# Kernel optimization log

Hardware: AMD Instinct MI355X
Metric: run time of the kernel (lower is better)

Reference implementation:

```python
import jax, jax.numpy as jnp
import numpy as np

N_NODES = 100000
N_EDGES = 1600000
D_IN = 128
HID = 128
E_CH = 16


def setup_inputs() -> dict:
    key = jax.random.key(0)
    ks = jax.random.split(key, 16)

    def glorot(k, shape):
        fan_in, fan_out = shape[0], shape[1]
        lim = jnp.sqrt(6.0 / (fan_in + fan_out))
        return jax.random.uniform(k, shape, jnp.float32, -lim, lim)

    inp = {
        "x": jax.random.normal(ks[0], (N_NODES, D_IN), jnp.float32),
        "edge_index": jax.random.randint(ks[1], (2, N_EDGES), 0, N_NODES, jnp.int32),
        "edge_attr": jax.random.normal(ks[2], (N_EDGES, E_CH), jnp.float32),
        # SAGEConv layer 0: lin_l (neighbor agg, with bias), lin_r (root, no bias)
        "Wl0": glorot(ks[3], (D_IN, HID)),
        "Wr0": glorot(ks[4], (D_IN, HID)),
        "b0": jnp.zeros((HID,), jnp.float32),
        # SAGEConv layer 1
        "Wl1": glorot(ks[5], (HID, HID)),
        "Wr1": glorot(ks[6], (HID, HID)),
        "b1": jnp.zeros((HID,), jnp.float32),
        # classifier MLP: (2*HID + E_CH) -> 128 -> 64 -> 1
        "Wc1": glorot(ks[7], (2 * HID + E_CH, 128)),
        "bc1": jnp.zeros((128,), jnp.float32),
        "Wc2": glorot(ks[8], (128, 64)),
        "bc2": jnp.zeros((64,), jnp.float32),
        "Wc3": glorot(ks[9], (64, 1)),
        "bc3": jnp.zeros((1,), jnp.float32),
    }
    return inp


def _sage_conv(x, src, dst, Wl, Wr, b):
    # PyG SAGEConv (aggr='mean'): out = lin_l(mean_j x_j) + lin_r(x_i)
    # messages flow src -> dst
    msg_sum = jax.ops.segment_sum(x[src], dst, num_segments=N_NODES)  # [N, D]
    deg = jax.ops.segment_sum(jnp.ones((src.shape[0],), x.dtype), dst,
                              num_segments=N_NODES)                   # [N]
    agg = msg_sum / jnp.maximum(deg, 1.0)[:, None]  # mean; isolated nodes -> 0
    return agg @ Wl + b + x @ Wr


def reference(x, edge_index, edge_attr,
              Wl0, Wr0, b0, Wl1, Wr1, b1,
              Wc1, bc1, Wc2, bc2, Wc3, bc3):
    src, dst = edge_index[0], edge_index[1]
    # encode: two SAGEConv layers, each followed by ReLU (dropout is identity at eval)
    h = jax.nn.relu(_sage_conv(x, src, dst, Wl0, Wr0, b0))
    h = jax.nn.relu(_sage_conv(h, src, dst, Wl1, Wr1, b1))
    # edge classifier: gather endpoint embeddings, concat edge features
    feat = jnp.concatenate([h[src], h[dst], edge_attr], axis=-1)  # [E, 2H+EC]
    z = jax.nn.relu(feat @ Wc1 + bc1)
    z = jax.nn.relu(z @ Wc2 + bc2)
    logits = (z @ Wc3 + bc3).reshape(-1)  # [E]
    return jax.nn.sigmoid(logits)
```

## Files before the change

### kernel.cpp

```cpp
#include <hip/hip_runtime.h>
#include <hip/hip_bf16.h>
#include <math.h>

#define NN 100000
#define NE 1600000
#define NBLK 391
#define ZSTRIDE 296

typedef __bf16 bf16x8 __attribute__((ext_vector_type(8)));
typedef float f32x4 __attribute__((ext_vector_type(4)));

union BF8 { bf16x8 v; unsigned short u[8]; };

static __device__ __forceinline__ unsigned short f2bf(float f) {
  unsigned int u = __float_as_uint(f);
  unsigned int r = u + 0x7fffu + ((u >> 16) & 1u);
  return (unsigned short)(r >> 16);
}
static __device__ __forceinline__ f32x4 zero4() {
  f32x4 z = {0.f, 0.f, 0.f, 0.f}; return z;
}
static __device__ __forceinline__ bf16x8 zerobf8() {
  BF8 t;
  #pragma unroll
  for (int j = 0; j < 8; ++j) t.u[j] = 0;
  return t.v;
}
static __device__ __forceinline__ bf16x8 cvt8(float4 v0, float4 v1, float s) {
  BF8 t;
  t.u[0]=f2bf(v0.x*s); t.u[1]=f2bf(v0.y*s); t.u[2]=f2bf(v0.z*s); t.u[3]=f2bf(v0.w*s);
  t.u[4]=f2bf(v1.x*s); t.u[5]=f2bf(v1.y*s); t.u[6]=f2bf(v1.z*s); t.u[7]=f2bf(v1.w*s);
  return t.v;
}

__global__ void prep_swizzle(const float* __restrict__ Wl0, const float* __restrict__ Wr0,
                             const float* __restrict__ Wl1, const float* __restrict__ Wr1,
                             const float* __restrict__ Wc1, const float* __restrict__ Wc2,
                             __hip_bfloat16* __restrict__ swz) {
  int gid = blockIdx.x * 256 + threadIdx.x;
  if (gid >= 110592) return;
  int id = gid;
  const float* A; const float* B = nullptr; int KC, Nc, Ksrc;
  if (id < 32768)        { KC = 8; Nc = 128; Ksrc = 256; A = Wl0; B = Wr0; }
  else if (id < 65536)   { id -= 32768; KC = 8; Nc = 128; Ksrc = 256; A = Wl1; B = Wr1; }
  else if (id < 102400)  { id -= 65536; KC = 9; Nc = 128; Ksrc = 272; A = Wc1; }
  else                   { id -= 102400; KC = 4; Nc = 64;  Ksrc = 128; A = Wc2; }
  int j = id & 7, lane = (id >> 3) & 63, rest = id >> 9;
  int c = rest % KC, t = rest / KC;
  int k = c * 32 + (lane >> 4) * 8 + j;
  int n = t * 16 + (lane & 15);
  float v = 0.f;
  if (k < Ksrc) {
    if (B && k >= 128) v = B[(k - 128) * Nc + n];
    else               v = A[k * Nc + n];
  }
  unsigned short* o = (unsigned short*)swz;
  o[gid] = f2bf(v);
}

__global__ void x_to_bf16(const float* __restrict__ x, __hip_bfloat16* __restrict__ xb) {
  int i = blockIdx.x * 256 + threadIdx.x;
  float4 v = ((const float4*)x)[i];
  ushort4 p;
  p.x = f2bf(v.x); p.y = f2bf(v.y); p.z = f2bf(v.z); p.w = f2bf(v.w);
  ((ushort4*)xb)[i] = p;
}

__global__ void deg_count(const int* __restrict__ ei, int* __restrict__ degCnt) {
  int e = blockIdx.x * 256 + threadIdx.x;
  atomicAdd(&degCnt[ei[NE + e]], 1);
}

__global__ void scan_block_sums(const int* __restrict__ degCnt, int* __restrict__ blockSums) {
  __shared__ int red[4];
  int i = blockIdx.x * 256 + threadIdx.x;
  int v = (i < NN) ? degCnt[i] : 0;
  #pragma unroll
  for (int off = 32; off; off >>= 1) v += __shfl_down(v, off, 64);
  if ((threadIdx.x & 63) == 0) red[threadIdx.x >> 6] = v;
  __syncthreads();
  if (threadIdx.x == 0) blockSums[blockIdx.x] = red[0] + red[1] + red[2] + red[3];
}

__global__ void scan_partials(const int* __restrict__ blockSums, int* __restrict__ blockOff) {
  __shared__ int lds[512];
  int t = threadIdx.x;
  int v = (t < NBLK) ? blockSums[t] : 0;
  lds[t] = v; __syncthreads();
  #pragma unroll
  for (int off = 1; off < 512; off <<= 1) {
    int a = (t >= off) ? lds[t - off] : 0;
    __syncthreads();
    lds[t] += a;
    __syncthreads();
  }
  if (t < NBLK) blockOff[t] = lds[t] - v;
}

__global__ void scan_write(const int* __restrict__ degCnt, const int* __restrict__ blockOff,
                           int* __restrict__ rowPtr, int* __restrict__ cursor) {
  __shared__ int lds[256];
  int t = threadIdx.x;
  int i = blockIdx.x * 256 + t;
  int v = (i < NN) ? degCnt[i] : 0;
  lds[t] = v; __syncthreads();
  #pragma unroll
  for (int off = 1; off < 256; off <<= 1) {
    int a = (t >= off) ? lds[t - off] : 0;
    __syncthreads();
    lds[t] += a;
    __syncthreads();
  }
  if (i < NN) {
    int excl = blockOff[blockIdx.x] + lds[t] - v;
    rowPtr[i] = excl;
    cursor[i] = excl;
  }
}

__global__ void csr_fill(const int* __restrict__ ei, int* __restrict__ cursor,
                         int* __restrict__ csrSrc) {
  int e = blockIdx.x * 256 + threadIdx.x;
  int s = ei[e], d = ei[NE + e];
  int idx = atomicAdd(&cursor[d], 1);
  csrSrc[idx] = s;
}

__global__ __launch_bounds__(256, 8)
void gather_agg(const __hip_bfloat16* __restrict__ xb,
                const int* __restrict__ csrSrc, const int* __restrict__ rowPtr,
                const int* __restrict__ degCnt, __hip_bfloat16* __restrict__ msgOut) {
  int n = blockIdx.x * 4 + (threadIdx.x >> 6);
  int lane = threadIdx.x & 63;
  int half = lane >> 5;
  int c4 = lane & 31;
  if (n >= NN) return;
  int rp = rowPtr[n], dg = degCnt[n];
  float a0 = 0.f, a1 = 0.f, a2 = 0.f, a3 = 0.f;
  for (int i = half; i < dg; i += 2) {
    int s = csrSrc[rp + i];
    uint2 u = *(const uint2*)((const unsigned short*)xb + (size_t)s * 128 + c4 * 4);
    a0 += __uint_as_float(u.x << 16);
    a1 += __uint_as_float(u.x & 0xffff0000u);
    a2 += __uint_as_float(u.y << 16);
    a3 += __uint_as_float(u.y & 0xffff0000u);
  }
  a0 += __shfl_xor(a0, 32);
  a1 += __shfl_xor(a1, 32);
  a2 += __shfl_xor(a2, 32);
  a3 += __shfl_xor(a3, 32);
  if (half == 0) {
    float r = 1.f / fmaxf((float)dg, 1.f);
    ushort4 p;
    p.x = f2bf(a0 * r); p.y = f2bf(a1 * r);
    p.z = f2bf(a2 * r); p.w = f2bf(a3 * r);
    *(ushort4*)((unsigned short*)msgOut + (size_t)n * 128 + c4 * 4) = p;
  }
}

__global__ __launch_bounds__(256, 2)
void node_gemm(const __hip_bfloat16* __restrict__ msgB,
               const __hip_bfloat16* __restrict__ selfB16,
               const __hip_bfloat16* __restrict__ swzW, const float* __restrict__ bias,
               __hip_bfloat16* __restrict__ hOut) {
  const int tid = threadIdx.x, w = tid >> 6, lane = tid & 63;
  const int l15 = lane & 15, quad = lane >> 4;
  const int nBase = blockIdx.x * 256 + w * 64;

  int row[4];
  #pragma unroll
  for (int t = 0; t < 4; ++t) {
    int n = nBase + t * 16 + l15;
    if (n > NN - 1) n = NN - 1;
    row[t] = n;
  }

  f32x4 acc[8][4];
  #pragma unroll
  for (int mt = 0; mt < 8; ++mt)
    #pragma unroll
    for (int nt = 0; nt < 4; ++nt) acc[mt][nt] = zero4();

  #pragma unroll
  for (int c = 0; c < 8; ++c) {
    bf16x8 bfr[4];
    if (c < 4) {
      #pragma unroll
      for (int nt = 0; nt < 4; ++nt)
        bfr[nt] = *(const bf16x8*)(msgB + (size_t)row[nt] * 128 + c * 32 + quad * 8);
    } else {
      #pragma unroll
      for (int nt = 0; nt < 4; ++nt)
        bfr[nt] = *(const bf16x8*)(selfB16 + (size_t)row[nt] * 128 + (c - 4) * 32 + quad * 8);
    }
    bf16x8 afr[8];
    #pragma unroll
    for (int mt = 0; mt < 8; ++mt)
      afr[mt] = *(const bf16x8*)(swzW + ((mt * 8 + c) * 64 + lane) * 8);
    #pragma unroll
    for (int mt = 0; mt < 8; ++mt)
      #pragma unroll
      for (int nt = 0; nt < 4; ++nt)
        acc[mt][nt] = __builtin_amdgcn_mfma_f32_16x16x32_bf16(afr[mt], bfr[nt], acc[mt][nt], 0, 0, 0);
  }

  #pragma unroll
  for (int mt = 0; mt < 8; ++mt) {
    const float4 b4 = *(const float4*)(bias + mt * 16 + quad * 4);
    #pragma unroll
    for (int nt = 0; nt < 4; ++nt) {
      int n = nBase + nt * 16 + l15;
      if (n < NN) {
        ushort4 p;
        p.x = f2bf(fmaxf(acc[mt][nt][0] + b4.x, 0.f));
        p.y = f2bf(fmaxf(acc[mt][nt][1] + b4.y, 0.f));
        p.z = f2bf(fmaxf(acc[mt][nt][2] + b4.z, 0.f));
        p.w = f2bf(fmaxf(acc[mt][nt][3] + b4.w, 0.f));
        *(ushort4*)(hOut + (size_t)n * 128 + mt * 16 + quad * 4) = p;
      }
    }
  }
}

__global__ __launch_bounds__(256, 4)
void edge_mlp(const __hip_bfloat16* __restrict__ h1, const int* __restrict__ ei,
              const float* __restrict__ ea,
              const __hip_bfloat16* __restrict__ swzWc1, const __hip_bfloat16* __restrict__ swzWc2,
              const float* __restrict__ Wc3, const float* __restrict__ bc1,
              const float* __restrict__ bc2, const float* __restrict__ bc3,
              float* __restrict__ out) {
  __shared__ char lds[4 * 32 * ZSTRIDE];
  const int tid = threadIdx.x, w = tid >> 6, lane = tid & 63;
  const int l15 = lane & 15, quad = lane >> 4;
  const int eBase = blockIdx.x * 128 + w * 32;
  char* zbuf = lds + w * (32 * ZSTRIDE);

  int eRow[2], srcOff[2], dstOff[2];
  #pragma unroll
  for (int t = 0; t < 2; ++t) {
    int e = eBase + t * 16 + l15;
    eRow[t] = e;
    srcOff[t] = ei[e] * 128;
    dstOff[t] = ei[NE + e] * 128;
  }

  f32x4 acc[8][2];
  #pragma unroll
  for (int mt = 0; mt < 8; ++mt)
    #pragma unroll
    for (int nt = 0; nt < 2; ++nt) acc[mt][nt] = zero4();

  #pragma unroll
  for (int c = 0; c < 9; ++c) {
    bf16x8 bfr[2];
    if (c < 4) {
      #pragma unroll
      for (int nt = 0; nt < 2; ++nt)
        bfr[nt] = *(const bf16x8*)(h1 + srcOff[nt] + c * 32 + quad * 8);
    } else if (c < 8) {
      #pragma unroll
      for (int nt = 0; nt < 2; ++nt)
        bfr[nt] = *(const bf16x8*)(h1 + dstOff[nt] + (c - 4) * 32 + quad * 8);
    } else {
      #pragma unroll
      for (int nt = 0; nt < 2; ++nt) {
        if (quad < 2) {
          const float4* p = (const float4*)(ea + (size_t)eRow[nt] * 16 + quad * 8);
          bfr[nt] = cvt8(p[0], p[1], 1.f);
        } else {
          bfr[nt] = zerobf8();
        }
      }
    }
    bf16x8 afr[8];
    #pragma unroll
    for (int mt = 0; mt < 8; ++mt)
      afr[mt] = *(const bf16x8*)(swzWc1 + ((mt * 9 + c) * 64 + lane) * 8);
    #pragma unroll
    for (int mt = 0; mt < 8; ++mt)
      #pragma unroll
      for (int nt = 0; nt < 2; ++nt)
        acc[mt][nt] = __builtin_amdgcn_mfma_f32_16x16x32_bf16(afr[mt], bfr[nt], acc[mt][nt], 0, 0, 0);
  }

  #pragma unroll
  for (int mt = 0; mt < 8; ++mt) {
    const float4 b4 = *(const float4*)(bc1 + mt * 16 + quad * 4);
    #pragma unroll
    for (int nt = 0; nt < 2; ++nt) {
      int er = nt * 16 + l15;
      ushort4 p;
      p.x = f2bf(fmaxf(acc[mt][nt][0] + b4.x, 0.f));
      p.y = f2bf(fmaxf(acc[mt][nt][1] + b4.y, 0.f));
      p.z = f2bf(fmaxf(acc[mt][nt][2] + b4.z, 0.f));
      p.w = f2bf(fmaxf(acc[mt][nt][3] + b4.w, 0.f));
      *(ushort4*)(zbuf + er * ZSTRIDE + (mt * 16 + quad * 4) * 2) = p;
    }
  }

  f32x4 acc2[4][2];
  #pragma unroll
  for (int mt = 0; mt < 4; ++mt)
    #pragma unroll
    for (int nt = 0; nt < 2; ++nt) acc2[mt][nt] = zero4();

  #pragma unroll
  for (int c = 0; c < 4; ++c) {
    bf16x8 bfr[2];
    #pragma unroll
    for (int nt = 0; nt < 2; ++nt)
      bfr[nt] = *(const bf16x8*)(zbuf + (nt * 16 + l15) * ZSTRIDE + (c * 32 + quad * 8) * 2);
    bf16x8 afr[4];
    #pragma unroll
    for (int mt = 0; mt < 4; ++mt)
      afr[mt] = *(const bf16x8*)(swzWc2 + ((mt * 4 + c) * 64 + lane) * 8);
    #pragma unroll
    for (int mt = 0; mt < 4; ++mt)
      #pragma unroll
      for (int nt = 0; nt < 2; ++nt)
        acc2[mt][nt] = __builtin_amdgcn_mfma_f32_16x16x32_bf16(afr[mt], bfr[nt], acc2[mt][nt], 0, 0, 0);
  }

  #pragma unroll
  for (int mt = 0; mt < 4; ++mt) {
    const float4 b4 = *(const float4*)(bc2 + mt * 16 + quad * 4);
    #pragma unroll
    for (int nt = 0; nt < 2; ++nt) {
      int er = nt * 16 + l15;
      ushort4 p;
      p.x = f2bf(fmaxf(acc2[mt][nt][0] + b4.x, 0.f));
      p.y = f2bf(fmaxf(acc2[mt][nt][1] + b4.y, 0.f));
      p.z = f2bf(fmaxf(acc2[mt][nt][2] + b4.z, 0.f));
      p.w = f2bf(fmaxf(acc2[mt][nt][3] + b4.w, 0.f));
      *(ushort4*)(zbuf + er * ZSTRIDE + (mt * 16 + quad * 4) * 2) = p;
    }
  }

  {
    int e = lane & 31, half = lane >> 5;
    float a3 = (half == 0) ? bc3[0] : 0.f;
    #pragma unroll
    for (int k2 = 0; k2 < 16; ++k2) {
      unsigned int u = *(const unsigned int*)(zbuf + e * ZSTRIDE + half * 64 + k2 * 4);
      float v0 = __uint_as_float(u << 16);
      float v1 = __uint_as_float(u & 0xffff0000u);
      const float2 wv = *(const float2*)(Wc3 + half * 32 + 2 * k2);
      a3 += v0 * wv.x + v1 * wv.y;
    }
    a3 += __shfl_xor(a3, 32);
    if (half == 0)
      out[eBase + e] = 1.f / (1.f + __expf(-a3));
  }
}

extern "C" void kernel_launch(void* const* d_in, const int* in_sizes, int n_in,
                              void* d_out, int out_size, void* d_ws, size_t ws_size,
                              hipStream_t stream) {
  const float* x   = (const float*)d_in[0];
  const int*   ei  = (const int*)d_in[1];
  const float* ea  = (const float*)d_in[2];
  const float* Wl0 = (const float*)d_in[3];
  const float* Wr0 = (const float*)d_in[4];
  const float* b0  = (const float*)d_in[5];
  const float* Wl1 = (const float*)d_in[6];
  const float* Wr1 = (const float*)d_in[7];
  const float* b1  = (const float*)d_in[8];
  const float* Wc1 = (const float*)d_in[9];
  const float* bc1 = (const float*)d_in[10];
  const float* Wc2 = (const float*)d_in[11];
  const float* bc2 = (const float*)d_in[12];
  const float* Wc3 = (const float*)d_in[13];
  const float* bc3 = (const float*)d_in[14];
  float* out = (float*)d_out;

  char* ws = (char*)d_ws;
  int* degCnt   = (int*)(ws + 0);
  int* rowPtr   = (int*)(ws + 400000);
  int* cursor   = (int*)(ws + 800000);
  int* blockSums= (int*)(ws + 1200000);
  int* blockOff = (int*)(ws + 1202048);
  int* csrSrc   = (int*)(ws + 1204096);
  __hip_bfloat16* msgB = (__hip_bfloat16*)(ws + 7604096);
  __hip_bfloat16* h0b  = (__hip_bfloat16*)(ws + 33204096);
  __hip_bfloat16* h1b  = (__hip_bfloat16*)(ws + 58804096);
  __hip_bfloat16* swz  = (__hip_bfloat16*)(ws + 84404096);
  __hip_bfloat16* xb = h1b;

  hipMemsetAsync(degCnt, 0, 400000, stream);
  prep_swizzle<<<432, 256, 0, stream>>>(Wl0, Wr0, Wl1, Wr1, Wc1, Wc2, swz);
  x_to_bf16<<<12500, 256, 0, stream>>>(x, xb);

  deg_count<<<NE / 256, 256, 0, stream>>>(ei, degCnt);
  scan_block_sums<<<NBLK, 256, 0, stream>>>(degCnt, blockSums);
  scan_partials<<<1, 512, 0, stream>>>(blockSums, blockOff);
  scan_write<<<NBLK, 256, 0, stream>>>(degCnt, blockOff, rowPtr, cursor);
  csr_fill<<<NE / 256, 256, 0, stream>>>(ei, cursor, csrSrc);

  gather_agg<<<NN / 4, 256, 0, stream>>>(xb, csrSrc, rowPtr, degCnt, msgB);
  node_gemm<<<(NN + 255) / 256, 256, 0, stream>>>(msgB, xb, swz, b0, h0b);

  gather_agg<<<NN / 4, 256, 0, stream>>>(h0b, csrSrc, rowPtr, degCnt, msgB);
  node_gemm<<<(NN + 255) / 256, 256, 0, stream>>>(msgB, h0b, swz + 32768, b1, h1b);

  edge_mlp<<<NE / 128, 256, 0, stream>>>(h1b, ei, ea, swz + 65536, swz + 102400,
                                         Wc3, bc1, bc2, bc3, out);
}
```

Before: 964.7 us.

## Precompute per-node Wc1 projections and process edges in CSR order

Splits the first classifier layer algebraically: h1@Wc1_src and h1@Wc1_dst are computed once per node in a new pq_gemm kernel (P and Q). The edge MLP then gathers the P/Q rows and adds them, leaving only the 16-wide edge_attr product per edge instead of a 272-deep GEMM. Edges are visited in dst-sorted CSR order, using a new csrDE array, for better locality on Q, and outputs are scattered back by the original edge id. gather_agg is also reworked to use 16 lanes per node with 16-byte loads and 4-way unrolling. Costs include an extra node GEMM, extra workspace, a scattered output write, and P/Q rounded to bf16 before summation.

```diff
diff --git a/kernel.cpp b/kernel.cpp
--- a/kernel.cpp
+++ b/kernel.cpp
@@ -5,7 +5,7 @@
 #define NN 100000
 #define NE 1600000
 #define NBLK 391
-#define ZSTRIDE 296
+#define ZS 296
 
 typedef __bf16 bf16x8 __attribute__((ext_vector_type(8)));
 typedef float f32x4 __attribute__((ext_vector_type(4)));
@@ -16,6 +16,9 @@
   unsigned int u = __float_as_uint(f);
   unsigned int r = u + 0x7fffu + ((u >> 16) & 1u);
   return (unsigned short)(r >> 16);
+}
+static __device__ __forceinline__ float bf2f(unsigned short b) {
+  return __uint_as_float((unsigned int)b << 16);
 }
 static __device__ __forceinline__ f32x4 zero4() {
   f32x4 z = {0.f, 0.f, 0.f, 0.f}; return z;
@@ -43,7 +46,9 @@
   const float* A; const float* B = nullptr; int KC, Nc, Ksrc;
   if (id < 32768)        { KC = 8; Nc = 128; Ksrc = 256; A = Wl0; B = Wr0; }
   else if (id < 65536)   { id -= 32768; KC = 8; Nc = 128; Ksrc = 256; A = Wl1; B = Wr1; }
-  else if (id < 102400)  { id -= 65536; KC = 9; Nc = 128; Ksrc = 272; A = Wc1; }
+  else if (id < 81920)   { id -= 65536; KC = 4; Nc = 128; Ksrc = 128; A = Wc1; }
+  else if (id < 98304)   { id -= 81920; KC = 4; Nc = 128; Ksrc = 128; A = Wc1 + 128 * 128; }
+  else if (id < 102400)  { id -= 98304; KC = 1; Nc = 128; Ksrc = 16;  A = Wc1 + 256 * 128; }
   else                   { id -= 102400; KC = 4; Nc = 64;  Ksrc = 128; A = Wc2; }
   int j = id & 7, lane = (id >> 3) & 63, rest = id >> 9;
   int c = rest % KC, t = rest / KC;
@@ -119,43 +124,45 @@
 }
 
 __global__ void csr_fill(const int* __restrict__ ei, int* __restrict__ cursor,
-                         int* __restrict__ csrSrc) {
+                         int* __restrict__ csrSrc, int2* __restrict__ csrDE) {
   int e = blockIdx.x * 256 + threadIdx.x;
   int s = ei[e], d = ei[NE + e];
   int idx = atomicAdd(&cursor[d], 1);
   csrSrc[idx] = s;
+  csrDE[idx] = make_int2(d, e);
 }
 
 __global__ __launch_bounds__(256, 8)
 void gather_agg(const __hip_bfloat16* __restrict__ xb,
                 const int* __restrict__ csrSrc, const int* __restrict__ rowPtr,
                 const int* __restrict__ degCnt, __hip_bfloat16* __restrict__ msgOut) {
-  int n = blockIdx.x * 4 + (threadIdx.x >> 6);
-  int lane = threadIdx.x & 63;
-  int half = lane >> 5;
-  int c4 = lane & 31;
-  if (n >= NN) return;
+  int g = threadIdx.x >> 4, c16 = threadIdx.x & 15;
+  int n = blockIdx.x * 16 + g;
   int rp = rowPtr[n], dg = degCnt[n];
-  float a0 = 0.f, a1 = 0.f, a2 = 0.f, a3 = 0.f;
-  for (int i = half; i < dg; i += 2) {
-    int s = csrSrc[rp + i];
-    uint2 u = *(const uint2*)((const unsigned short*)xb + (size_t)s * 128 + c4 * 4);
-    a0 += __uint_as_float(u.x << 16);
-    a1 += __uint_as_float(u.x & 0xffff0000u);
-    a2 += __uint_as_float(u.y << 16);
-    a3 += __uint_as_float(u.y & 0xffff0000u);
-  }
-  a0 += __shfl_xor(a0, 32);
-  a1 += __shfl_xor(a1, 32);
-  a2 += __shfl_xor(a2, 32);
-  a3 += __shfl_xor(a3, 32);
-  if (half == 0) {
-    float r = 1.f / fmaxf((float)dg, 1.f);
-    ushort4 p;
-    p.x = f2bf(a0 * r); p.y = f2bf(a1 * r);
-    p.z = f2bf(a2 * r); p.w = f2bf(a3 * r);
-    *(ushort4*)((unsigned short*)msgOut + (size_t)n * 128 + c4 * 4) = p;
-  }
+  float a[8];
+  #pragma unroll
+  for (int j = 0; j < 8; ++j) a[j] = 0.f;
+  for (int i = 0; i < dg; i += 4) {
+    #pragma unroll
+    for (int k = 0; k < 4; ++k) {
+      int ii = i + k;
+      int s = csrSrc[rp + (ii < dg ? ii : dg - 1)];
+      uint4 u = *(const uint4*)((const unsigned short*)xb + (size_t)s * 128 + c16 * 8);
+      if (ii < dg) {
+        a[0] += bf2f((unsigned short)(u.x & 0xffff)); a[1] += bf2f((unsigned short)(u.x >> 16));
+        a[2] += bf2f((unsigned short)(u.y & 0xffff)); a[3] += bf2f((unsigned short)(u.y >> 16));
+        a[4] += bf2f((unsigned short)(u.z & 0xffff)); a[5] += bf2f((unsigned short)(u.z >> 16));
+        a[6] += bf2f((unsigned short)(u.w & 0xffff)); a[7] += bf2f((unsigned short)(u.w >> 16));
+      }
+    }
+  }
+  float r = 1.f / fmaxf((float)dg, 1.f);
+  uint4 p;
+  p.x = (unsigned)f2bf(a[0] * r) | ((unsigned)f2bf(a[1] * r) << 16);
+  p.y = (unsigned)f2bf(a[2] * r) | ((unsigned)f2bf(a[3] * r) << 16);
+  p.z = (unsigned)f2bf(a[4] * r) | ((unsigned)f2bf(a[5] * r) << 16);
+  p.w = (unsigned)f2bf(a[6] * r) | ((unsigned)f2bf(a[7] * r) << 16);
+  *(uint4*)((unsigned short*)msgOut + (size_t)n * 128 + c16 * 8) = p;
 }
 
 __global__ __launch_bounds__(256, 2)
@@ -222,26 +229,85 @@
   }
 }
 
+__global__ __launch_bounds__(256, 2)
+void pq_gemm(const __hip_bfloat16* __restrict__ h1, const __hip_bfloat16* __restrict__ swzPQ,
+             __hip_bfloat16* __restrict__ Pout, __hip_bfloat16* __restrict__ Qout) {
+  const __hip_bfloat16* swzW = swzPQ + blockIdx.y * 16384;
+  __hip_bfloat16* outp = blockIdx.y ? Qout : Pout;
+  const int tid = threadIdx.x, w = tid >> 6, lane = tid & 63;
+  const int l15 = lane & 15, quad = lane >> 4;
+  const int nBase = blockIdx.x * 256 + w * 64;
+
+  int row[4];
+  #pragma unroll
+  for (int t = 0; t < 4; ++t) {
+    int n = nBase + t * 16 + l15;
+    if (n > NN - 1) n = NN - 1;
+    row[t] = n;
+  }
+
+  f32x4 acc[8][4];
+  #pragma unroll
+  for (int mt = 0; mt < 8; ++mt)
+    #pragma unroll
+    for (int nt = 0; nt < 4; ++nt) acc[mt][nt] = zero4();
+
+  #pragma unroll
+  for (int c = 0; c < 4; ++c) {
+    bf16x8 bfr[4];
+    #pragma unroll
+    for (int nt = 0; nt < 4; ++nt)
+      bfr[nt] = *(const bf16x8*)(h1 + (size_t)row[nt] * 128 + c * 32 + quad * 8);
+    bf16x8 afr[8];
+    #pragma unroll
+    for (int mt = 0; mt < 8; ++mt)
+      afr[mt] = *(const bf16x8*)(swzW + ((mt * 4 + c) * 64 + lane) * 8);
+    #pragma unroll
+    for (int mt = 0; mt < 8; ++mt)
+      #pragma unroll
+      for (int nt = 0; nt < 4; ++nt)
+        acc[mt][nt] = __builtin_amdgcn_mfma_f32_16x16x32_bf16(afr[mt], bfr[nt], acc[mt][nt], 0, 0, 0);
+  }
+
+  #pragma unroll
+  for (int mt = 0; mt < 8; ++mt) {
+    #pragma unroll
+    for (int nt = 0; nt < 4; ++nt) {
+      int n = nBase + nt * 16 + l15;
+      if (n < NN) {
+        ushort4 p;
+        p.x = f2bf(acc[mt][nt][0]);
+        p.y = f2bf(acc[mt][nt][1]);
+        p.z = f2bf(acc[mt][nt][2]);
+        p.w = f2bf(acc[mt][nt][3]);
+        *(ushort4*)(outp + (size_t)n * 128 + mt * 16 + quad * 4) = p;
+      }
+    }
+  }
+}
+
 __global__ __launch_bounds__(256, 4)
-void edge_mlp(const __hip_bfloat16* __restrict__ h1, const int* __restrict__ ei,
+void edge_mlp(const __hip_bfloat16* __restrict__ P, const __hip_bfloat16* __restrict__ Q,
               const float* __restrict__ ea,
-              const __hip_bfloat16* __restrict__ swzWc1, const __hip_bfloat16* __restrict__ swzWc2,
+              const int* __restrict__ csrSrc, const int2* __restrict__ csrDE,
+              const __hip_bfloat16* __restrict__ swzWea, const __hip_bfloat16* __restrict__ swzWc2,
               const float* __restrict__ Wc3, const float* __restrict__ bc1,
               const float* __restrict__ bc2, const float* __restrict__ bc3,
               float* __restrict__ out) {
-  __shared__ char lds[4 * 32 * ZSTRIDE];
+  __shared__ char lds[4 * 32 * ZS];
   const int tid = threadIdx.x, w = tid >> 6, lane = tid & 63;
   const int l15 = lane & 15, quad = lane >> 4;
   const int eBase = blockIdx.x * 128 + w * 32;
-  char* zbuf = lds + w * (32 * ZSTRIDE);
-
-  int eRow[2], srcOff[2], dstOff[2];
+  char* zbuf = lds + w * (32 * ZS);
+
+  int srcO[2], dstO[2], eid[2];
   #pragma unroll
   for (int t = 0; t < 2; ++t) {
-    int e = eBase + t * 16 + l15;
-    eRow[t] = e;
-    srcOff[t] = ei[e] * 128;
-    dstOff[t] = ei[NE + e] * 128;
+    int p = eBase + t * 16 + l15;
+    srcO[t] = csrSrc[p] * 128;
+    int2 de = csrDE[p];
+    dstO[t] = de.x * 128;
+    eid[t] = de.y;
   }
 
   f32x4 acc[8][2];
@@ -250,89 +316,76 @@
     #pragma unroll
     for (int nt = 0; nt < 2; ++nt) acc[mt][nt] = zero4();
 
-  #pragma unroll
-  for (int c = 0; c < 9; ++c) {
-    bf16x8 bfr[2];
-    if (c < 4) {
+  bf16x8 bfr[2];
+  #pragma unroll
+  for (int nt = 0; nt < 2; ++nt) {
+    if (quad < 2) {
+      const float4* pe = (const float4*)(ea + (size_t)eid[nt] * 16 + quad * 8);
+      bfr[nt] = cvt8(pe[0], pe[1], 1.f);
+    } else {
+      bfr[nt] = zerobf8();
+    }
+  }
+  #pragma unroll
+  for (int mt = 0; mt < 8; ++mt) {
+    bf16x8 afr = *(const bf16x8*)(swzWea + (mt * 64 + lane) * 8);
+    #pragma unroll
+    for (int nt = 0; nt < 2; ++nt)
+      acc[mt][nt] = __builtin_amdgcn_mfma_f32_16x16x32_bf16(afr, bfr[nt], acc[mt][nt], 0, 0, 0);
+  }
+
+  #pragma unroll
+  for (int mt = 0; mt < 8; ++mt) {
+    const int cb = mt * 16 + quad * 4;
+    const float4 b4 = *(const float4*)(bc1 + cb);
+    #pragma unroll
+    for (int nt = 0; nt < 2; ++nt) {
+      ushort4 pu = *(const ushort4*)(P + srcO[nt] + cb);
+      ushort4 qu = *(const ushort4*)(Q + dstO[nt] + cb);
+      int er = nt * 16 + l15;
+      ushort4 z;
+      z.x = f2bf(fmaxf(acc[mt][nt][0] + bf2f(pu.x) + bf2f(qu.x) + b4.x, 0.f));
+      z.y = f2bf(fmaxf(acc[mt][nt][1] + bf2f(pu.y) + bf2f(qu.y) + b4.y, 0.f));
+      z.z = f2bf(fmaxf(acc[mt][nt][2] + bf2f(pu.z) + bf2f(qu.z) + b4.z, 0.f));
+      z.w = f2bf(fmaxf(acc[mt][nt][3] + bf2f(pu.w) + bf2f(qu.w) + b4.w, 0.f));
+      *(ushort4*)(zbuf + er * ZS + cb * 2) = z;
+    }
+  }
+
+  f32x4 acc2[4][2];
+  #pragma unroll
+  for (int mt = 0; mt < 4; ++mt)
+    #pragma unroll
+    for (int nt = 0; nt < 2; ++nt) acc2[mt][nt] = zero4();
+
+  #pragma unroll
+  for (int c = 0; c < 4; ++c) {
+    bf16x8 b2[2];
+    #pragma unroll
+    for (int nt = 0; nt < 2; ++nt)
+      b2[nt] = *(const bf16x8*)(zbuf + (nt * 16 + l15) * ZS + (c * 32 + quad * 8) * 2);
+    #pragma unroll
+    for (int mt = 0; mt < 4; ++mt) {
+      bf16x8 afr = *(const bf16x8*)(swzWc2 + ((mt * 4 + c) * 64 + lane) * 8);
       #pragma unroll
       for (int nt = 0; nt < 2; ++nt)
-        bfr[nt] = *(const bf16x8*)(h1 + srcOff[nt] + c * 32 + quad * 8);
-    } else if (c < 8) {
-      #pragma unroll
-      for (int nt = 0; nt < 2; ++nt)
-        bfr[nt] = *(const bf16x8*)(h1 + dstOff[nt] + (c - 4) * 32 + quad * 8);
-    } else {
-      #pragma unroll
-      for (int nt = 0; nt < 2; ++nt) {
-        if (quad < 2) {
-          const float4* p = (const float4*)(ea + (size_t)eRow[nt] * 16 + quad * 8);
-          bfr[nt] = cvt8(p[0], p[1], 1.f);
-        } else {
-          bfr[nt] = zerobf8();
-        }
-      }
-    }
-    bf16x8 afr[8];
-    #pragma unroll
-    for (int mt = 0; mt < 8; ++mt)
-      afr[mt] = *(const bf16x8*)(swzWc1 + ((mt * 9 + c) * 64 + lane) * 8);
-    #pragma unroll
-    for (int mt = 0; mt < 8; ++mt)
-      #pragma unroll
-      for (int nt = 0; nt < 2; ++nt)
-        acc[mt][nt] = __builtin_amdgcn_mfma_f32_16x16x32_bf16(afr[mt], bfr[nt], acc[mt][nt], 0, 0, 0);
-  }
-
-  #pragma unroll
-  for (int mt = 0; mt < 8; ++mt) {
-    const float4 b4 = *(const float4*)(bc1 + mt * 16 + quad * 4);
+        acc2[mt][nt] = __builtin_amdgcn_mfma_f32_16x16x32_bf16(afr, b2[nt], acc2[mt][nt], 0, 0, 0);
+    }
+  }
+
+  #pragma unroll
+  for (int mt = 0; mt < 4; ++mt) {
+    const int cb = mt * 16 + quad * 4;
+    const float4 b4 = *(const float4*)(bc2 + cb);
     #pragma unroll
     for (int nt = 0; nt < 2; ++nt) {
       int er = nt * 16 + l15;
-      ushort4 p;
-      p.x = f2bf(fmaxf(acc[mt][nt][0] + b4.x, 0.f));
-      p.y = f2bf(fmaxf(acc[mt][nt][1] + b4.y, 0.f));
-      p.z = f2bf(fmaxf(acc[mt][nt][2] + b4.z, 0.f));
-      p.w = f2bf(fmaxf(acc[mt][nt][3] + b4.w, 0.f));
-      *(ushort4*)(zbuf + er * ZSTRIDE + (mt * 16 + quad * 4) * 2) = p;
-    }
-  }
-
-  f32x4 acc2[4][2];
-  #pragma unroll
-  for (int mt = 0; mt < 4; ++mt)
-    #pragma unroll
-    for (int nt = 0; nt < 2; ++nt) acc2[mt][nt] = zero4();
-
-  #pragma unroll
-  for (int c = 0; c < 4; ++c) {
-    bf16x8 bfr[2];
-    #pragma unroll
-    for (int nt = 0; nt < 2; ++nt)
-      bfr[nt] = *(const bf16x8*)(zbuf + (nt * 16 + l15) * ZSTRIDE + (c * 32 + quad * 8) * 2);
-    bf16x8 afr[4];
-    #pragma unroll
-    for (int mt = 0; mt < 4; ++mt)
-      afr[mt] = *(const bf16x8*)(swzWc2 + ((mt * 4 + c) * 64 + lane) * 8);
-    #pragma unroll
-    for (int mt = 0; mt < 4; ++mt)
-      #pragma unroll
-      for (int nt = 0; nt < 2; ++nt)
-        acc2[mt][nt] = __builtin_amdgcn_mfma_f32_16x16x32_bf16(afr[mt], bfr[nt], acc2[mt][nt], 0, 0, 0);
-  }
-
-  #pragma unroll
-  for (int mt = 0; mt < 4; ++mt) {
-    const float4 b4 = *(const float4*)(bc2 + mt * 16 + quad * 4);
-    #pragma unroll
-    for (int nt = 0; nt < 2; ++nt) {
-      int er = nt * 16 + l15;
-      ushort4 p;
-      p.x = f2bf(fmaxf(acc2[mt][nt][0] + b4.x, 0.f));
-      p.y = f2bf(fmaxf(acc2[mt][nt][1] + b4.y, 0.f));
-      p.z = f2bf(fmaxf(acc2[mt][nt][2] + b4.z, 0.f));
-      p.w = f2bf(fmaxf(acc2[mt][nt][3] + b4.w, 0.f));
-      *(ushort4*)(zbuf + er * ZSTRIDE + (mt * 16 + quad * 4) * 2) = p;
+      ushort4 z;
+      z.x = f2bf(fmaxf(acc2[mt][nt][0] + b4.x, 0.f));
+      z.y = f2bf(fmaxf(acc2[mt][nt][1] + b4.y, 0.f));
+      z.z = f2bf(fmaxf(acc2[mt][nt][2] + b4.z, 0.f));
+      z.w = f2bf(fmaxf(acc2[mt][nt][3] + b4.w, 0.f));
+      *(ushort4*)(zbuf + er * ZS + cb * 2) = z;
     }
   }
 
@@ -341,15 +394,17 @@
     float a3 = (half == 0) ? bc3[0] : 0.f;
     #pragma unroll
     for (int k2 = 0; k2 < 16; ++k2) {
-      unsigned int u = *(const unsigned int*)(zbuf + e * ZSTRIDE + half * 64 + k2 * 4);
+      unsigned int u = *(const unsigned int*)(zbuf + e * ZS + half * 64 + k2 * 4);
       float v0 = __uint_as_float(u << 16);
       float v1 = __uint_as_float(u & 0xffff0000u);
       const float2 wv = *(const float2*)(Wc3 + half * 32 + 2 * k2);
       a3 += v0 * wv.x + v1 * wv.y;
     }
     a3 += __shfl_xor(a3, 32);
-    if (half == 0)
-      out[eBase + e] = 1.f / (1.f + __expf(-a3));
+    if (half == 0) {
+      int oe = csrDE[eBase + e].y;
+      out[oe] = 1.f / (1.f + __expf(-a3));
+    }
   }
 }
 
@@ -374,17 +429,20 @@
   float* out = (float*)d_out;
 
   char* ws = (char*)d_ws;
-  int* degCnt   = (int*)(ws + 0);
-  int* rowPtr   = (int*)(ws + 400000);
-  int* cursor   = (int*)(ws + 800000);
-  int* blockSums= (int*)(ws + 1200000);
-  int* blockOff = (int*)(ws + 1202048);
-  int* csrSrc   = (int*)(ws + 1204096);
-  __hip_bfloat16* msgB = (__hip_bfloat16*)(ws + 7604096);
-  __hip_bfloat16* h0b  = (__hip_bfloat16*)(ws + 33204096);
-  __hip_bfloat16* h1b  = (__hip_bfloat16*)(ws + 58804096);
-  __hip_bfloat16* swz  = (__hip_bfloat16*)(ws + 84404096);
-  __hip_bfloat16* xb = h1b;
+  int* degCnt    = (int*)(ws + 0);
+  int* rowPtr    = (int*)(ws + 400000);
+  int* cursor    = (int*)(ws + 800000);
+  int* blockSums = (int*)(ws + 1200000);
+  int* blockOff  = (int*)(ws + 1202048);
+  int* csrSrc    = (int*)(ws + 1204096);
+  int2* csrDE    = (int2*)(ws + 7604096);
+  __hip_bfloat16* bufB = (__hip_bfloat16*)(ws + 20404096);
+  __hip_bfloat16* bufC = (__hip_bfloat16*)(ws + 46004096);
+  __hip_bfloat16* bufD = (__hip_bfloat16*)(ws + 71604096);
+  __hip_bfloat16* swz  = (__hip_bfloat16*)(ws + 97204096);
+  __hip_bfloat16* msgB = bufB; __hip_bfloat16* Pb = bufB;
+  __hip_bfloat16* h0b  = bufC; __hip_bfloat16* Qb = bufC;
+  __hip_bfloat16* xb   = bufD; __hip_bfloat16* h1b = bufD;
 
   hipMemsetAsync(degCnt, 0, 400000, stream);
   prep_swizzle<<<432, 256, 0, stream>>>(Wl0, Wr0, Wl1, Wr1, Wc1, Wc2, swz);
@@ -394,14 +452,16 @@
   scan_block_sums<<<NBLK, 256, 0, stream>>>(degCnt, blockSums);
   scan_partials<<<1, 512, 0, stream>>>(blockSums, blockOff);
   scan_write<<<NBLK, 256, 0, stream>>>(degCnt, blockOff, rowPtr, cursor);
-  csr_fill<<<NE / 256, 256, 0, stream>>>(ei, cursor, csrSrc);
-
-  gather_agg<<<NN / 4, 256, 0, stream>>>(xb, csrSrc, rowPtr, degCnt, msgB);
-  node_gemm<<<(NN + 255) / 256, 256, 0, stream>>>(msgB, xb, swz, b0, h0b);
-
-  gather_agg<<<NN / 4, 256, 0, stream>>>(h0b, csrSrc, rowPtr, degCnt, msgB);
-  node_gemm<<<(NN + 255) / 256, 256, 0, stream>>>(msgB, h0b, swz + 32768, b1, h1b);
-
-  edge_mlp<<<NE / 128, 256, 0, stream>>>(h1b, ei, ea, swz + 65536, swz + 102400,
+  csr_fill<<<NE / 256, 256, 0, stream>>>(ei, cursor, csrSrc, csrDE);
+
+  gather_agg<<<NN / 16, 256, 0, stream>>>(xb, csrSrc, rowPtr, degCnt, msgB);
+  node_gemm<<<NBLK, 256, 0, stream>>>(msgB, xb, swz, b0, h0b);
+
+  gather_agg<<<NN / 16, 256, 0, stream>>>(h0b, csrSrc, rowPtr, degCnt, msgB);
+  node_gemm<<<NBLK, 256, 0, stream>>>(msgB, h0b, swz + 32768, b1, h1b);
+
+  pq_gemm<<<dim3(NBLK, 2), 256, 0, stream>>>(h1b, swz + 65536, Pb, Qb);
+  edge_mlp<<<NE / 128, 256, 0, stream>>>(Pb, Qb, ea, csrSrc, csrDE,
+                                         swz + 98304, swz + 102400,
                                          Wc3, bc1, bc2, bc3, out);
 }
```

Result: faster. 859.3 us (-10.9%).
